# Optimization experiments

Hardware: AMD Instinct MI355X
Metric: run time of the kernel (lower is better)

The kernel has to match this reference:

```python
import jax, jax.numpy as jnp
import numpy as np

D = 512      # d_model
H = 8        # n_heads
NB = 6       # n_blocks
V = 32000    # vocab
F = 2048     # ff_size
B, L = 2, 1024
EPS = 1e-6
NEG = -1e10  # -INF used by create_causal_bias


def _ln(x, g, b):
    m = jnp.mean(x, axis=-1, keepdims=True)
    v = jnp.mean((x - m) ** 2, axis=-1, keepdims=True)
    return (x - m) * jax.lax.rsqrt(v + EPS) * g + b


def _split_heads(t):
    b, l, _ = t.shape
    return t.reshape(b, l, H, D // H).transpose(0, 2, 1, 3)  # [B,H,L,dh]


def _mha(q_in, kv_in, bias, wq, wk, wv, wo):
    # manual q@k^T / sqrt(dh) + bias -> softmax -> @v -> out proj (no bias terms)
    q = _split_heads(q_in @ wq)
    k = _split_heads(kv_in @ wk)
    v = _split_heads(kv_in @ wv)
    s = jnp.einsum('bhqd,bhkd->bhqk', q, k) / (D // H) ** 0.5 + bias
    a = jax.nn.softmax(s, axis=-1)
    o = jnp.einsum('bhqk,bhkd->bhqd', a, v)
    b_, _, l, _ = o.shape
    o = o.transpose(0, 2, 1, 3).reshape(b_, l, D)
    return o @ wo


def _pos_enc(length):
    pos = jnp.arange(length, dtype=jnp.float32)
    half = D // 2
    i = jnp.arange(half, dtype=jnp.float32)
    scaled = pos[:, None] / jnp.power(10000.0, i / half)[None]
    return jnp.concatenate([jnp.sin(scaled), jnp.cos(scaled)], axis=1)  # [L, D]


def setup_inputs() -> dict:
    key = jax.random.key(0)
    ks = jax.random.split(key, 16)
    s = 0.02
    inp = {
        'x': jax.random.randint(ks[0], (B, L), 0, V, dtype=jnp.int32),
        'ctx': jax.random.normal(ks[1], (B, L, D), jnp.float32),
        'emb': jax.random.normal(ks[2], (V, D), jnp.float32) * s,
        'wq_s': jax.random.normal(ks[3], (NB, D, D), jnp.float32) * s,
        'wk_s': jax.random.normal(ks[4], (NB, D, D), jnp.float32) * s,
        'wv_s': jax.random.normal(ks[5], (NB, D, D), jnp.float32) * s,
        'wo_s': jax.random.normal(ks[6], (NB, D, D), jnp.float32) * s,
        'wq_c': jax.random.normal(ks[7], (NB, D, D), jnp.float32) * s,
        'wk_c': jax.random.normal(ks[8], (NB, D, D), jnp.float32) * s,
        'wv_c': jax.random.normal(ks[9], (NB, D, D), jnp.float32) * s,
        'wo_c': jax.random.normal(ks[10], (NB, D, D), jnp.float32) * s,
        'w1': jax.random.normal(ks[11], (NB, D, F), jnp.float32) * s,
        'b1': jnp.zeros((NB, F), jnp.float32),
        'w2': jax.random.normal(ks[12], (NB, F, D), jnp.float32) * s,
        'b2': jnp.zeros((NB, D), jnp.float32),
        'ln1_g': jnp.ones((NB, D), jnp.float32), 'ln1_b': jnp.zeros((NB, D), jnp.float32),
        'ln2_g': jnp.ones((NB, D), jnp.float32), 'ln2_b': jnp.zeros((NB, D), jnp.float32),
        'ln3_g': jnp.ones((NB, D), jnp.float32), 'ln3_b': jnp.zeros((NB, D), jnp.float32),
        'lnf_g': jnp.ones((D,), jnp.float32), 'lnf_b': jnp.zeros((D,), jnp.float32),
    }
    return inp


def reference(x, ctx, emb, wq_s, wk_s, wv_s, wo_s, wq_c, wk_c, wv_c, wo_c,
              w1, b1, w2, b2, ln1_g, ln1_b, ln2_g, ln2_b, ln3_g, ln3_b,
              lnf_g, lnf_b):
    length = x.shape[1]
    # embedding * sqrt(D) + sinusoidal positional encoding
    h = emb[x] * jnp.sqrt(jnp.float32(D)) + _pos_enc(length)[None]
    # causal bias: upper triangle (excl. diag) filled with -INF, shape [1,1,L,L]
    causal = ((1.0 - jnp.tril(jnp.ones((length, length), jnp.float32))) * NEG)[None, None]
    zero_bias = jnp.zeros((1, 1, 1, 1), jnp.float32)  # no masking of encoder ctx
    for i in range(NB):
        y = _ln(h, ln1_g[i], ln1_b[i])
        h = h + _mha(y, y, causal, wq_s[i], wk_s[i], wv_s[i], wo_s[i])
        y = _ln(h, ln2_g[i], ln2_b[i])
        h = h + _mha(y, ctx, zero_bias, wq_c[i], wk_c[i], wv_c[i], wo_c[i])
        y = _ln(h, ln3_g[i], ln3_b[i])
        h = h + (jax.nn.relu(y @ w1[i] + b1[i]) @ w2[i] + b2[i])
    h = _ln(h, lnf_g, lnf_b)
    # emb2logits: shared embedding projection
    return jnp.einsum('bld,vd->blv', h, emb)
```

## Files before the change

### kernel.cpp

```cpp
#include <hip/hip_runtime.h>
#include <math.h>

#define Bv 2
#define Lv 1024
#define Dv 512
#define Hv 8
#define DH 64
#define Fv 2048
#define NBv 6
#define Vv 32000
#define Mv (Bv*Lv)
#define QS 1536
#define NEGINF -1e10f

typedef __attribute__((ext_vector_type(8))) short short8;
typedef __attribute__((ext_vector_type(4))) short short4v;
typedef __attribute__((ext_vector_type(4))) float floatx4;
typedef __attribute__((address_space(1))) const void gvoid;
typedef __attribute__((address_space(3))) void svoid;

__device__ __forceinline__ short f2bf(float f) {
    union { float f; unsigned u; } v; v.f = f;
    unsigned r = v.u + 0x7fffu + ((v.u >> 16) & 1u);
    return (short)(r >> 16);
}

__global__ __launch_bounds__(256)
void embed_kernel(const int* __restrict__ xi, const float* __restrict__ emb,
                  float* __restrict__ h)
{
    const int row = blockIdx.x;
    const int l   = row & (Lv - 1);
    const int tok = xi[row];
    const int tid = threadIdx.x;
#pragma unroll
    for (int s = 0; s < 2; ++s) {
        const int d  = tid + s * 256;
        const int dd = d & 255;
        const float freq = powf(10000.f, (float)dd * (1.f / 256.f));
        const float arg  = (float)l / freq;
        const float pe   = (d < 256) ? sinf(arg) : cosf(arg);
        h[(size_t)row * Dv + d] = emb[(size_t)tok * Dv + d] * 22.62741699796952f + pe;
    }
}

__global__ __launch_bounds__(256)
void cvt_kernel(const float* __restrict__ X, short* __restrict__ Y)
{
    const int i = (blockIdx.x * 256 + threadIdx.x) * 4;
    const float4 v = *(const float4*)(X + i);
    short4v p; p.x = f2bf(v.x); p.y = f2bf(v.y); p.z = f2bf(v.z); p.w = f2bf(v.w);
    *(short4v*)(Y + i) = p;
}

__global__ __launch_bounds__(256)
void ln_kernel(const float* __restrict__ X, const float* __restrict__ g,
               const float* __restrict__ bta, short* __restrict__ Y)
{
    const int row = blockIdx.x, tid = threadIdx.x;
    const float* xr = X + (size_t)row * Dv;
    const float x0 = xr[tid], x1 = xr[tid + 256];
    __shared__ float red[4];

    float s = x0 + x1;
#pragma unroll
    for (int off = 32; off; off >>= 1) s += __shfl_xor(s, off);
    if ((tid & 63) == 0) red[tid >> 6] = s;
    __syncthreads();
    const float mean = (red[0] + red[1] + red[2] + red[3]) * (1.f / Dv);
    __syncthreads();

    const float d0 = x0 - mean, d1 = x1 - mean;
    float v = d0 * d0 + d1 * d1;
#pragma unroll
    for (int off = 32; off; off >>= 1) v += __shfl_xor(v, off);
    if ((tid & 63) == 0) red[tid >> 6] = v;
    __syncthreads();
    const float var  = (red[0] + red[1] + red[2] + red[3]) * (1.f / Dv);
    const float rstd = rsqrtf(var + 1e-6f);

    Y[(size_t)row * Dv + tid]       = f2bf(d0 * rstd * g[tid]       + bta[tid]);
    Y[(size_t)row * Dv + tid + 256] = f2bf(d1 * rstd * g[tid + 256] + bta[tid + 256]);
}

template <int BM, int BN, int BK, int BMODE, bool OUTBF, bool SWZ>
__global__ __launch_bounds__(256)
void mgemm(const short* __restrict__ A, const float* __restrict__ B,
           void* __restrict__ Cp, int M, int N, int K,
           const float* __restrict__ bias,
           const float* __restrict__ residual, int relu)
{
    constexpr int WMT = BM / 2, MI = WMT / 16, NF = BN / 32;
    constexpr int CPR = BK / 8;
    __shared__ short As[BM * BK];
    __shared__ short Bs[BN * BK];
    const int tid  = threadIdx.x;
    const int wave = tid >> 6, lane = tid & 63;
    const int wm = wave & 1, wn = wave >> 1;
    const int quad = lane >> 4, l16 = lane & 15;

    int m0, n0;
    if (SWZ) {
        const int wg = (blockIdx.x & 7) * 500 + (blockIdx.x >> 3);
        m0 = (wg & 15) * BM;
        n0 = (wg >> 4) * BN;
    } else {
        m0 = blockIdx.y * BM;
        n0 = blockIdx.x * BN;
    }

    floatx4 acc[MI][NF];
#pragma unroll
    for (int i = 0; i < MI; ++i)
#pragma unroll
        for (int j = 0; j < NF; ++j)
            acc[i][j] = (floatx4){0.f, 0.f, 0.f, 0.f};

    for (int k0 = 0; k0 < K; k0 += BK) {
        __syncthreads();
#pragma unroll
        for (int s = 0; s < (BM * CPR) / 256; ++s) {
            const int c = s * 256 + tid;
            const int row = c / CPR, kp = (c % CPR) * 8;
            const int kps = kp ^ ((row & 7) << 3);
            const short* gp = A + (size_t)(m0 + row) * K + k0 + kps;
            __builtin_amdgcn_global_load_lds((gvoid*)gp, (svoid*)((char*)As + c * 16),
                                             16, 0, 0);
        }
        if (BMODE == 0) {
            constexpr int QN = BN / 4;
            constexpr int KSTEP = (256 / QN) * 4;
            const int qn  = tid % QN;
            const int kq0 = (tid / QN) * 4;
#pragma unroll
            for (int p = 0; p < BK / KSTEP; ++p) {
                const int krow = p * KSTEP + kq0;
                const float* gp = B + (size_t)(k0 + krow) * N + n0 + qn * 4;
                const float4 r0 = *(const float4*)(gp);
                const float4 r1 = *(const float4*)(gp + N);
                const float4 r2 = *(const float4*)(gp + 2 * (size_t)N);
                const float4 r3 = *(const float4*)(gp + 3 * (size_t)N);
#pragma unroll
                for (int e = 0; e < 4; ++e) {
                    const int n = qn * 4 + e;
                    short4v p4;
                    p4.x = f2bf(e == 0 ? r0.x : e == 1 ? r0.y : e == 2 ? r0.z : r0.w);
                    p4.y = f2bf(e == 0 ? r1.x : e == 1 ? r1.y : e == 2 ? r1.z : r1.w);
                    p4.z = f2bf(e == 0 ? r2.x : e == 1 ? r2.y : e == 2 ? r2.z : r2.w);
                    p4.w = f2bf(e == 0 ? r3.x : e == 1 ? r3.y : e == 2 ? r3.z : r3.w);
                    *(short4v*)&Bs[n * BK + (krow ^ ((n & 7) << 3))] = p4;
                }
            }
        } else if (BMODE == 1) {
#pragma unroll
            for (int f = 0; f < (BN * (BK / 4)) / 256; ++f) {
                const int gidx = f * 256 + tid;
                const int n = gidx / (BK / 4), q = (gidx % (BK / 4)) * 4;
                const float4 r = *(const float4*)(B + (size_t)(n0 + n) * K + k0 + q);
                short4v p; p.x = f2bf(r.x); p.y = f2bf(r.y); p.z = f2bf(r.z); p.w = f2bf(r.w);
                *(short4v*)&Bs[n * BK + (q ^ ((n & 7) << 3))] = p;
            }
        } else {
            const short* Bb = (const short*)B;
#pragma unroll
            for (int s = 0; s < (BN * CPR) / 256; ++s) {
                const int c = s * 256 + tid;
                const int row = c / CPR, kp = (c % CPR) * 8;
                const int kps = kp ^ ((row & 7) << 3);
                const short* gp = Bb + (size_t)(n0 + row) * K + k0 + kps;
                __builtin_amdgcn_global_load_lds((gvoid*)gp, (svoid*)((char*)Bs + c * 16),
                                                 16, 0, 0);
            }
        }
        __syncthreads();
#pragma unroll
        for (int kk = 0; kk < BK; kk += 32) {
            short8 af[MI];
#pragma unroll
            for (int mi = 0; mi < MI; ++mi) {
                const int r = wm * WMT + mi * 16 + l16;
                af[mi] = *(short8*)&As[r * BK + ((kk + quad * 8) ^ ((r & 7) << 3))];
            }
#pragma unroll
            for (int ni = 0; ni < NF; ++ni) {
                const int n = wn * (BN / 2) + ni * 16 + l16;
                const short8 bfr = *(short8*)&Bs[n * BK + ((kk + quad * 8) ^ ((n & 7) << 3))];
#pragma unroll
                for (int mi = 0; mi < MI; ++mi)
                    acc[mi][ni] = __builtin_amdgcn_mfma_f32_16x16x32_bf16(af[mi], bfr, acc[mi][ni], 0, 0, 0);
            }
        }
    }

#pragma unroll
    for (int mi = 0; mi < MI; ++mi)
#pragma unroll
        for (int ni = 0; ni < NF; ++ni)
#pragma unroll
            for (int r = 0; r < 4; ++r) {
                const int m = m0 + wm * WMT + mi * 16 + quad * 4 + r;
                const int n = n0 + wn * (BN / 2) + ni * 16 + l16;
                float v = acc[mi][ni][r];
                if (bias)     v += bias[n];
                if (residual) v += residual[(size_t)m * N + n];
                if (relu)     v = fmaxf(v, 0.f);
                if (OUTBF) ((short*)Cp)[(size_t)m * N + n] = f2bf(v);
                else       ((float*)Cp)[(size_t)m * N + n] = v;
            }
}

__global__ __launch_bounds__(256)
void qkv_gemm(const short* __restrict__ Aq, const short* __restrict__ Akv,
              const float* __restrict__ B0, const float* __restrict__ B1,
              const float* __restrict__ B2, short* __restrict__ QKV)
{
    constexpr int BM = 64, BN = 64, BK = 64, N = Dv, K = Dv;
    constexpr int WMT = BM / 2, MI = WMT / 16, NF = 2;
    constexpr int CPR = BK / 8;
    __shared__ short As[BM * BK];
    __shared__ short Bs[BN * BK];
    const int tid  = threadIdx.x;
    const int wave = tid >> 6, lane = tid & 63;
    const int wm = wave & 1, wn = wave >> 1;
    const int quad = lane >> 4, l16 = lane & 15;
    const int n0g = blockIdx.x * BN, m0 = blockIdx.y * BM;
    const int wsel = n0g >> 9, n0 = n0g & 511;
    const short* A = (wsel == 0) ? Aq : Akv;
    const float* B = (wsel == 0) ? B0 : (wsel == 1) ? B1 : B2;

    floatx4 acc[MI][NF];
#pragma unroll
    for (int i = 0; i < MI; ++i)
#pragma unroll
        for (int j = 0; j < NF; ++j)
            acc[i][j] = (floatx4){0.f, 0.f, 0.f, 0.f};

    for (int k0 = 0; k0 < K; k0 += BK) {
        __syncthreads();
#pragma unroll
        for (int s = 0; s < (BM * CPR) / 256; ++s) {
            const int c = s * 256 + tid;
            const int row = c / CPR, kp = (c % CPR) * 8;
            const int kps = kp ^ ((row & 7) << 3);
            const short* gp = A + (size_t)(m0 + row) * K + k0 + kps;
            __builtin_amdgcn_global_load_lds((gvoid*)gp, (svoid*)((char*)As + c * 16),
                                             16, 0, 0);
        }
        {
            constexpr int QN = BN / 4;
            const int qn  = tid % QN;
            const int krow = (tid / QN) * 4;
            const float* gp = B + (size_t)(k0 + krow) * N + n0 + qn * 4;
            const float4 r0 = *(const float4*)(gp);
            const float4 r1 = *(const float4*)(gp + N);
            const float4 r2 = *(const float4*)(gp + 2 * (size_t)N);
            const float4 r3 = *(const float4*)(gp + 3 * (size_t)N);
#pragma unroll
            for (int e = 0; e < 4; ++e) {
                const int n = qn * 4 + e;
                short4v p4;
                p4.x = f2bf(e == 0 ? r0.x : e == 1 ? r0.y : e == 2 ? r0.z : r0.w);
                p4.y = f2bf(e == 0 ? r1.x : e == 1 ? r1.y : e == 2 ? r1.z : r1.w);
                p4.z = f2bf(e == 0 ? r2.x : e == 1 ? r2.y : e == 2 ? r2.z : r2.w);
                p4.w = f2bf(e == 0 ? r3.x : e == 1 ? r3.y : e == 2 ? r3.z : r3.w);
                *(short4v*)&Bs[n * BK + (krow ^ ((n & 7) << 3))] = p4;
            }
        }
        __syncthreads();
#pragma unroll
        for (int kk = 0; kk < BK; kk += 32) {
            short8 af[MI];
#pragma unroll
            for (int mi = 0; mi < MI; ++mi) {
                const int r = wm * WMT + mi * 16 + l16;
                af[mi] = *(short8*)&As[r * BK + ((kk + quad * 8) ^ ((r & 7) << 3))];
            }
#pragma unroll
            for (int ni = 0; ni < NF; ++ni) {
                const int n = wn * 32 + ni * 16 + l16;
                const short8 bfr = *(short8*)&Bs[n * BK + ((kk + quad * 8) ^ ((n & 7) << 3))];
#pragma unroll
                for (int mi = 0; mi < MI; ++mi)
                    acc[mi][ni] = __builtin_amdgcn_mfma_f32_16x16x32_bf16(af[mi], bfr, acc[mi][ni], 0, 0, 0);
            }
        }
    }

#pragma unroll
    for (int mi = 0; mi < MI; ++mi)
#pragma unroll
        for (int ni = 0; ni < NF; ++ni)
#pragma unroll
            for (int r = 0; r < 4; ++r) {
                const int m = m0 + wm * WMT + mi * 16 + quad * 4 + r;
                const int n = n0g + wn * 32 + ni * 16 + l16;
                QKV[(size_t)m * QS + n] = f2bf(acc[mi][ni][r]);
            }
}

__global__ __launch_bounds__(256)
void attn_mfma(const short* __restrict__ QKV, short* __restrict__ Op, int causal)
{
    constexpr int PK = 72;
    __shared__ short Ks[64 * PK];
    __shared__ short Vs[64 * PK];
    __shared__ short Ps[4][16 * PK];
    const int tid  = threadIdx.x;
    const int wave = tid >> 6, lane = tid & 63;
    const int quad = lane >> 4, l16 = lane & 15;
    const int hh = blockIdx.y, bb = blockIdx.z;
    const int q0 = blockIdx.x * 64;
    const size_t base  = (size_t)bb * Lv * QS + (size_t)hh * DH;
    const short* Qp = QKV + base;
    const short* Kp = QKV + base + 512;
    const short* Vp = QKV + base + 1024;
    const size_t obase = (size_t)bb * Lv * Dv + (size_t)hh * DH;

    short8 aq[2];
    {
        const short* qp = Qp + (size_t)(q0 + wave * 16 + l16) * QS + quad * 8;
        aq[0] = *(const short8*)qp;
        aq[1] = *(const short8*)(qp + 32);
    }

    floatx4 o[4];
#pragma unroll
    for (int i = 0; i < 4; ++i) o[i] = (floatx4){0.f, 0.f, 0.f, 0.f};
    float mrow[4] = {-3.4e38f, -3.4e38f, -3.4e38f, -3.4e38f};
    float srow[4] = {0.f, 0.f, 0.f, 0.f};

    const int ntiles = causal ? (q0 / 64 + 1) : (Lv / 64);

    for (int t = 0; t < ntiles; ++t) {
        const int j0 = t * 64;
        __syncthreads();
#pragma unroll
        for (int s = 0; s < 2; ++s) {
            const int c = s * 256 + tid;
            const int j = c >> 3, off = (c & 7) * 8;
            const size_t grow = (size_t)(j0 + j) * QS + off;
            *(short8*)&Ks[j * PK + off] = *(const short8*)(Kp + grow);
            const short8 v = *(const short8*)(Vp + grow);
            const int jx = j ^ ((c & 7) << 3);
#pragma unroll
            for (int e = 0; e < 8; ++e)
                Vs[(off + e) * PK + jx] = v[e];
        }
        __syncthreads();

        floatx4 sf[4];
#pragma unroll
        for (int nf = 0; nf < 4; ++nf) {
            const short8 bk0 = *(const short8*)&Ks[(nf * 16 + l16) * PK + quad * 8];
            const short8 bk1 = *(const short8*)&Ks[(nf * 16 + l16) * PK + 32 + quad * 8];
            floatx4 z = (floatx4){0.f, 0.f, 0.f, 0.f};
            z = __builtin_amdgcn_mfma_f32_16x16x32_bf16(aq[0], bk0, z, 0, 0, 0);
            z = __builtin_amdgcn_mfma_f32_16x16x32_bf16(aq[1], bk1, z, 0, 0, 0);
            sf[nf] = z;
        }

        const bool mask = causal && (j0 == q0);
#pragma unroll
        for (int nf = 0; nf < 4; ++nf) {
            const int jabs = j0 + nf * 16 + l16;
#pragma unroll
            for (int r = 0; r < 4; ++r) {
                float v = sf[nf][r] * 0.125f;
                if (mask && jabs > q0 + wave * 16 + quad * 4 + r) v = NEGINF;
                sf[nf][r] = v;
            }
        }

#pragma unroll
        for (int r = 0; r < 4; ++r) {
            float v = fmaxf(fmaxf(sf[0][r], sf[1][r]), fmaxf(sf[2][r], sf[3][r]));
            v = fmaxf(v, __shfl_xor(v, 1));
            v = fmaxf(v, __shfl_xor(v, 2));
            v = fmaxf(v, __shfl_xor(v, 4));
            v = fmaxf(v, __shfl_xor(v, 8));
            const float mnew = fmaxf(mrow[r], v);
            const float corr = __expf(mrow[r] - mnew);
            mrow[r] = mnew;
            srow[r] *= corr;
#pragma unroll
            for (int nf = 0; nf < 4; ++nf) o[nf][r] *= corr;
        }

#pragma unroll
        for (int nf = 0; nf < 4; ++nf) {
#pragma unroll
            for (int r = 0; r < 4; ++r) {
                const float pv = __expf(sf[nf][r] - mrow[r]);
                srow[r] += pv;
                Ps[wave][(quad * 4 + r) * PK + nf * 16 + l16] = f2bf(pv);
            }
        }
        __builtin_amdgcn_wave_barrier();

        const short8 pa0 = *(const short8*)&Ps[wave][l16 * PK + quad * 8];
        const short8 pa1 = *(const short8*)&Ps[wave][l16 * PK + 32 + quad * 8];
#pragma unroll
        for (int nf = 0; nf < 4; ++nf) {
            const int d   = nf * 16 + l16;
            const int swz = ((d >> 3) & 7) << 3;
            const short8 bv0 = *(const short8*)&Vs[d * PK + ((quad * 8) ^ swz)];
            const short8 bv1 = *(const short8*)&Vs[d * PK + ((32 + quad * 8) ^ swz)];
            o[nf] = __builtin_amdgcn_mfma_f32_16x16x32_bf16(pa0, bv0, o[nf], 0, 0, 0);
            o[nf] = __builtin_amdgcn_mfma_f32_16x16x32_bf16(pa1, bv1, o[nf], 0, 0, 0);
        }
    }

#pragma unroll
    for (int r = 0; r < 4; ++r) {
        float s = srow[r];
        s += __shfl_xor(s, 1);
        s += __shfl_xor(s, 2);
        s += __shfl_xor(s, 4);
        s += __shfl_xor(s, 8);
        srow[r] = 1.f / s;
    }
#pragma unroll
    for (int nf = 0; nf < 4; ++nf)
#pragma unroll
        for (int r = 0; r < 4; ++r) {
            const size_t addr = obase + (size_t)(q0 + wave * 16 + quad * 4 + r) * Dv
                              + nf * 16 + l16;
            Op[addr] = f2bf(o[nf][r] * srow[r]);
        }
}

extern "C" void kernel_launch(void* const* d_in, const int* in_sizes, int n_in,
                              void* d_out, int out_size, void* d_ws, size_t ws_size,
                              hipStream_t stream)
{
    const int*   x    = (const int*)  d_in[0];
    const float* ctx  = (const float*)d_in[1];
    const float* emb  = (const float*)d_in[2];
    const float* wq_s = (const float*)d_in[3];
    const float* wk_s = (const float*)d_in[4];
    const float* wv_s = (const float*)d_in[5];
    const float* wo_s = (const float*)d_in[6];
    const float* wq_c = (const float*)d_in[7];
    const float* wk_c = (const float*)d_in[8];
    const float* wv_c = (const float*)d_in[9];
    const float* wo_c = (const float*)d_in[10];
    const float* w1   = (const float*)d_in[11];
    const float* b1   = (const float*)d_in[12];
    const float* w2   = (const float*)d_in[13];
    const float* b2   = (const float*)d_in[14];
    const float* ln1g = (const float*)d_in[15];
    const float* ln1b = (const float*)d_in[16];
    const float* ln2g = (const float*)d_in[17];
    const float* ln2b = (const float*)d_in[18];
    const float* ln3g = (const float*)d_in[19];
    const float* ln3b = (const float*)d_in[20];
    const float* lnfg = (const float*)d_in[21];
    const float* lnfb = (const float*)d_in[22];
    float* out = (float*)d_out;

    char* wsb = (char*)d_ws;
    float* h      = (float*)(wsb);
    short* y_bf   = (short*)(wsb + (4u  << 20));
    short* ao_bf  = (short*)(wsb + (6u  << 20));
    short* ctx_bf = (short*)(wsb + (8u  << 20));
    short* qkv    = (short*)(wsb + (10u << 20));
    short* ff_bf  = (short*)(wsb + (10u << 20));
    short* emb_bf = (short*)(wsb + (18u << 20));
    const bool fastv = ws_size >= (52u << 20);

    const dim3 blk(256);
    const dim3 gAttn(Lv / 64, Hv, Bv);
    const dim3 gQKV(QS / 64, Mv / 64);
    const dim3 gD(Dv / 64, Mv / 32);
    const dim3 gF(Fv / 128, Mv / 64);
    const dim3 gV(16 * 250);

    embed_kernel<<<Mv, blk, 0, stream>>>(x, emb, h);
    cvt_kernel<<<(Mv * Dv) / 1024, blk, 0, stream>>>(ctx, ctx_bf);
    if (fastv)
        cvt_kernel<<<(Vv * Dv) / 1024, blk, 0, stream>>>(emb, emb_bf);

    for (int i = 0; i < NBv; ++i) {
        const size_t wOff = (size_t)i * Dv * Dv;
        ln_kernel<<<Mv, blk, 0, stream>>>(h, ln1g + i * Dv, ln1b + i * Dv, y_bf);
        qkv_gemm<<<gQKV, blk, 0, stream>>>(y_bf, y_bf,
                                           wq_s + wOff, wk_s + wOff, wv_s + wOff, qkv);
        attn_mfma<<<gAttn, blk, 0, stream>>>(qkv, ao_bf, 1);
        mgemm<32, 64, 64, 0, false, false><<<gD, blk, 0, stream>>>(ao_bf, wo_s + wOff, h,
                                                                   Mv, Dv, Dv, nullptr, h, 0);
        ln_kernel<<<Mv, blk, 0, stream>>>(h, ln2g + i * Dv, ln2b + i * Dv, y_bf);
        qkv_gemm<<<gQKV, blk, 0, stream>>>(y_bf, ctx_bf,
                                           wq_c + wOff, wk_c + wOff, wv_c + wOff, qkv);
        attn_mfma<<<gAttn, blk, 0, stream>>>(qkv, ao_bf, 0);
        mgemm<32, 64, 64, 0, false, false><<<gD, blk, 0, stream>>>(ao_bf, wo_c + wOff, h,
                                                                   Mv, Dv, Dv, nullptr, h, 0);
        ln_kernel<<<Mv, blk, 0, stream>>>(h, ln3g + i * Dv, ln3b + i * Dv, y_bf);
        mgemm<64, 128, 64, 0, true, false><<<gF, blk, 0, stream>>>(y_bf, w1 + (size_t)i * Dv * Fv,
                                                                   ff_bf, Mv, Fv, Dv,
                                                                   b1 + (size_t)i * Fv, nullptr, 1);
        mgemm<32, 64, 64, 0, false, false><<<gD, blk, 0, stream>>>(ff_bf, w2 + (size_t)i * Fv * Dv,
                                                                   h, Mv, Dv, Fv,
                                                                   b2 + (size_t)i * Dv, h, 0);
    }

    ln_kernel<<<Mv, blk, 0, stream>>>(h, lnfg, lnfb, y_bf);
    if (fastv)
        mgemm<128, 128, 64, 2, false, true><<<gV, blk, 0, stream>>>(y_bf, (const float*)emb_bf,
                                                                    out, Mv, Vv, Dv,
                                                                    nullptr, nullptr, 0);
    else
        mgemm<128, 128, 64, 1, false, true><<<gV, blk, 0, stream>>>(y_bf, emb, out,
                                                                    Mv, Vv, Dv,
                                                                    nullptr, nullptr, 0);
}
```

Before: 1.671 ms.

## Pre-transpose weights to bf16, batch cross-attention KV projection, double-buffer GEMM loads

When the workspace is large enough, all weights are converted once per call to transposed bf16, so every GEMM uses the direct global-to-LDS bf16 load path instead of converting fp32 B tiles in-kernel. The cross-attention K/V projections for all six blocks are computed in one large GEMM up front, since ctx does not change between blocks. The bf16 path also gains a double-buffered LDS pipeline that overlaps the next tile's loads with MFMA compute. The cost is extra transpose launches each call and a much larger workspace, and if the workspace is too small the old path runs instead.

```diff
diff --git a/kernel.cpp b/kernel.cpp
--- a/kernel.cpp
+++ b/kernel.cpp
@@ -11,6 +11,7 @@
 #define Vv 32000
 #define Mv (Bv*Lv)
 #define QS 1536
+#define KVS 6144
 #define NEGINF -1e10f
 
 typedef __attribute__((ext_vector_type(8))) short short8;
@@ -54,6 +55,35 @@
 }
 
 __global__ __launch_bounds__(256)
+void tr_cvt(const float* __restrict__ src, short* __restrict__ dst,
+            int K, int N, size_t dstZ, size_t dstOff)
+{
+    __shared__ float t[64][65];
+    const int z  = blockIdx.z;
+    const int n0 = blockIdx.x * 64, k0 = blockIdx.y * 64;
+    const int tid = threadIdx.x;
+    const float* s = src + (size_t)z * K * N;
+    short* d = dst + (size_t)z * dstZ + dstOff;
+
+    const int kr = tid >> 2, nc = (tid & 3) * 16;
+#pragma unroll
+    for (int j = 0; j < 16; j += 4) {
+        const float4 v = *(const float4*)(s + (size_t)(k0 + kr) * N + n0 + nc + j);
+        t[kr][nc + j + 0] = v.x; t[kr][nc + j + 1] = v.y;
+        t[kr][nc + j + 2] = v.z; t[kr][nc + j + 3] = v.w;
+    }
+    __syncthreads();
+    const int nr = tid >> 2, kc = (tid & 3) * 16;
+    short8 o0, o1;
+#pragma unroll
+    for (int j = 0; j < 8; ++j)  o0[j] = f2bf(t[kc + j][nr]);
+#pragma unroll
+    for (int j = 0; j < 8; ++j)  o1[j] = f2bf(t[kc + 8 + j][nr]);
+    *(short8*)(d + (size_t)(n0 + nr) * K + k0 + kc)     = o0;
+    *(short8*)(d + (size_t)(n0 + nr) * K + k0 + kc + 8) = o1;
+}
+
+__global__ __launch_bounds__(256)
 void ln_kernel(const float* __restrict__ X, const float* __restrict__ g,
                const float* __restrict__ bta, short* __restrict__ Y)
 {
@@ -83,7 +113,7 @@
     Y[(size_t)row * Dv + tid + 256] = f2bf(d1 * rstd * g[tid + 256] + bta[tid + 256]);
 }
 
-template <int BM, int BN, int BK, int BMODE, bool OUTBF, bool SWZ>
+template <int BM, int BN, int BK, int BMODE, bool OUTBF, bool SWZ, bool DBUF>
 __global__ __launch_bounds__(256)
 void mgemm(const short* __restrict__ A, const float* __restrict__ B,
            void* __restrict__ Cp, int M, int N, int K,
@@ -92,8 +122,9 @@
 {
     constexpr int WMT = BM / 2, MI = WMT / 16, NF = BN / 32;
     constexpr int CPR = BK / 8;
-    __shared__ short As[BM * BK];
-    __shared__ short Bs[BN * BK];
+    constexpr int NBUF = (DBUF && BMODE == 2) ? 2 : 1;
+    __shared__ short As[NBUF * BM * BK];
+    __shared__ short Bs[NBUF * BN * BK];
     const int tid  = threadIdx.x;
     const int wave = tid >> 6, lane = tid & 63;
     const int wm = wave & 1, wn = wave >> 1;
@@ -116,79 +147,116 @@
         for (int j = 0; j < NF; ++j)
             acc[i][j] = (floatx4){0.f, 0.f, 0.f, 0.f};
 
-    for (int k0 = 0; k0 < K; k0 += BK) {
-        __syncthreads();
-#pragma unroll
-        for (int s = 0; s < (BM * CPR) / 256; ++s) {
-            const int c = s * 256 + tid;
-            const int row = c / CPR, kp = (c % CPR) * 8;
-            const int kps = kp ^ ((row & 7) << 3);
-            const short* gp = A + (size_t)(m0 + row) * K + k0 + kps;
-            __builtin_amdgcn_global_load_lds((gvoid*)gp, (svoid*)((char*)As + c * 16),
-                                             16, 0, 0);
-        }
-        if (BMODE == 0) {
-            constexpr int QN = BN / 4;
-            constexpr int KSTEP = (256 / QN) * 4;
-            const int qn  = tid % QN;
-            const int kq0 = (tid / QN) * 4;
-#pragma unroll
-            for (int p = 0; p < BK / KSTEP; ++p) {
-                const int krow = p * KSTEP + kq0;
-                const float* gp = B + (size_t)(k0 + krow) * N + n0 + qn * 4;
-                const float4 r0 = *(const float4*)(gp);
-                const float4 r1 = *(const float4*)(gp + N);
-                const float4 r2 = *(const float4*)(gp + 2 * (size_t)N);
-                const float4 r3 = *(const float4*)(gp + 3 * (size_t)N);
-#pragma unroll
-                for (int e = 0; e < 4; ++e) {
-                    const int n = qn * 4 + e;
-                    short4v p4;
-                    p4.x = f2bf(e == 0 ? r0.x : e == 1 ? r0.y : e == 2 ? r0.z : r0.w);
-                    p4.y = f2bf(e == 0 ? r1.x : e == 1 ? r1.y : e == 2 ? r1.z : r1.w);
-                    p4.z = f2bf(e == 0 ? r2.x : e == 1 ? r2.y : e == 2 ? r2.z : r2.w);
-                    p4.w = f2bf(e == 0 ? r3.x : e == 1 ? r3.y : e == 2 ? r3.z : r3.w);
-                    *(short4v*)&Bs[n * BK + (krow ^ ((n & 7) << 3))] = p4;
-                }
-            }
-        } else if (BMODE == 1) {
-#pragma unroll
-            for (int f = 0; f < (BN * (BK / 4)) / 256; ++f) {
-                const int gidx = f * 256 + tid;
-                const int n = gidx / (BK / 4), q = (gidx % (BK / 4)) * 4;
-                const float4 r = *(const float4*)(B + (size_t)(n0 + n) * K + k0 + q);
-                short4v p; p.x = f2bf(r.x); p.y = f2bf(r.y); p.z = f2bf(r.z); p.w = f2bf(r.w);
-                *(short4v*)&Bs[n * BK + (q ^ ((n & 7) << 3))] = p;
-            }
-        } else {
-            const short* Bb = (const short*)B;
+    auto computeTile = [&](const short* Asb, const short* Bsb) {
+#pragma unroll
+        for (int kk = 0; kk < BK; kk += 32) {
+            short8 af[MI];
+#pragma unroll
+            for (int mi = 0; mi < MI; ++mi) {
+                const int r = wm * WMT + mi * 16 + l16;
+                af[mi] = *(const short8*)&Asb[r * BK + ((kk + quad * 8) ^ ((r & 7) << 3))];
+            }
+#pragma unroll
+            for (int ni = 0; ni < NF; ++ni) {
+                const int n = wn * (BN / 2) + ni * 16 + l16;
+                const short8 bfr = *(const short8*)&Bsb[n * BK + ((kk + quad * 8) ^ ((n & 7) << 3))];
+#pragma unroll
+                for (int mi = 0; mi < MI; ++mi)
+                    acc[mi][ni] = __builtin_amdgcn_mfma_f32_16x16x32_bf16(af[mi], bfr, acc[mi][ni], 0, 0, 0);
+            }
+        }
+    };
+
+    if constexpr (DBUF && BMODE == 2) {
+        const short* Bb = (const short*)B;
+        auto stage = [&](int buf, int kbase) {
+#pragma unroll
+            for (int s = 0; s < (BM * CPR) / 256; ++s) {
+                const int c = s * 256 + tid;
+                const int row = c / CPR, kp = (c % CPR) * 8;
+                const int kps = kp ^ ((row & 7) << 3);
+                const short* gp = A + (size_t)(m0 + row) * K + kbase + kps;
+                __builtin_amdgcn_global_load_lds((gvoid*)gp,
+                    (svoid*)((char*)As + buf * (BM * BK * 2) + c * 16), 16, 0, 0);
+            }
 #pragma unroll
             for (int s = 0; s < (BN * CPR) / 256; ++s) {
                 const int c = s * 256 + tid;
                 const int row = c / CPR, kp = (c % CPR) * 8;
                 const int kps = kp ^ ((row & 7) << 3);
-                const short* gp = Bb + (size_t)(n0 + row) * K + k0 + kps;
-                __builtin_amdgcn_global_load_lds((gvoid*)gp, (svoid*)((char*)Bs + c * 16),
+                const short* gp = Bb + (size_t)(n0 + row) * K + kbase + kps;
+                __builtin_amdgcn_global_load_lds((gvoid*)gp,
+                    (svoid*)((char*)Bs + buf * (BN * BK * 2) + c * 16), 16, 0, 0);
+            }
+        };
+        stage(0, 0);
+        __syncthreads();
+        const int NT = K / BK;
+        for (int t = 0; t < NT; ++t) {
+            const int cur = t & 1;
+            if (t + 1 < NT) stage(cur ^ 1, (t + 1) * BK);
+            computeTile(As + cur * BM * BK, Bs + cur * BN * BK);
+            __syncthreads();
+        }
+    } else {
+        for (int k0 = 0; k0 < K; k0 += BK) {
+            __syncthreads();
+#pragma unroll
+            for (int s = 0; s < (BM * CPR) / 256; ++s) {
+                const int c = s * 256 + tid;
+                const int row = c / CPR, kp = (c % CPR) * 8;
+                const int kps = kp ^ ((row & 7) << 3);
+                const short* gp = A + (size_t)(m0 + row) * K + k0 + kps;
+                __builtin_amdgcn_global_load_lds((gvoid*)gp, (svoid*)((char*)As + c * 16),
                                                  16, 0, 0);
             }
-        }
-        __syncthreads();
-#pragma unroll
-        for (int kk = 0; kk < BK; kk += 32) {
-            short8 af[MI];
-#pragma unroll
-            for (int mi = 0; mi < MI; ++mi) {
-                const int r = wm * WMT + mi * 16 + l16;
-                af[mi] = *(short8*)&As[r * BK + ((kk + quad * 8) ^ ((r & 7) << 3))];
-            }
-#pragma unroll
-            for (int ni = 0; ni < NF; ++ni) {
-                const int n = wn * (BN / 2) + ni * 16 + l16;
-                const short8 bfr = *(short8*)&Bs[n * BK + ((kk + quad * 8) ^ ((n & 7) << 3))];
-#pragma unroll
-                for (int mi = 0; mi < MI; ++mi)
-                    acc[mi][ni] = __builtin_amdgcn_mfma_f32_16x16x32_bf16(af[mi], bfr, acc[mi][ni], 0, 0, 0);
-            }
+            if (BMODE == 0) {
+                constexpr int QN = BN / 4;
+                constexpr int KSTEP = (256 / QN) * 4;
+                const int qn  = tid % QN;
+                const int kq0 = (tid / QN) * 4;
+#pragma unroll
+                for (int p = 0; p < BK / KSTEP; ++p) {
+                    const int krow = p * KSTEP + kq0;
+                    const float* gp = B + (size_t)(k0 + krow) * N + n0 + qn * 4;
+                    const float4 r0 = *(const float4*)(gp);
+                    const float4 r1 = *(const float4*)(gp + N);
+                    const float4 r2 = *(const float4*)(gp + 2 * (size_t)N);
+                    const float4 r3 = *(const float4*)(gp + 3 * (size_t)N);
+#pragma unroll
+                    for (int e = 0; e < 4; ++e) {
+                        const int n = qn * 4 + e;
+                        short4v p4;
+                        p4.x = f2bf(e == 0 ? r0.x : e == 1 ? r0.y : e == 2 ? r0.z : r0.w);
+                        p4.y = f2bf(e == 0 ? r1.x : e == 1 ? r1.y : e == 2 ? r1.z : r1.w);
+                        p4.z = f2bf(e == 0 ? r2.x : e == 1 ? r2.y : e == 2 ? r2.z : r2.w);
+                        p4.w = f2bf(e == 0 ? r3.x : e == 1 ? r3.y : e == 2 ? r3.z : r3.w);
+                        *(short4v*)&Bs[n * BK + (krow ^ ((n & 7) << 3))] = p4;
+                    }
+                }
+            } else if (BMODE == 1) {
+#pragma unroll
+                for (int f = 0; f < (BN * (BK / 4)) / 256; ++f) {
+                    const int gidx = f * 256 + tid;
+                    const int n = gidx / (BK / 4), q = (gidx % (BK / 4)) * 4;
+                    const float4 r = *(const float4*)(B + (size_t)(n0 + n) * K + k0 + q);
+                    short4v p; p.x = f2bf(r.x); p.y = f2bf(r.y); p.z = f2bf(r.z); p.w = f2bf(r.w);
+                    *(short4v*)&Bs[n * BK + (q ^ ((n & 7) << 3))] = p;
+                }
+            } else {
+                const short* Bb = (const short*)B;
+#pragma unroll
+                for (int s = 0; s < (BN * CPR) / 256; ++s) {
+                    const int c = s * 256 + tid;
+                    const int row = c / CPR, kp = (c % CPR) * 8;
+                    const int kps = kp ^ ((row & 7) << 3);
+                    const short* gp = Bb + (size_t)(n0 + row) * K + k0 + kps;
+                    __builtin_amdgcn_global_load_lds((gvoid*)gp, (svoid*)((char*)Bs + c * 16),
+                                                     16, 0, 0);
+                }
+            }
+            __syncthreads();
+            computeTile(As, Bs);
         }
     }
 
@@ -299,7 +367,9 @@
 }
 
 __global__ __launch_bounds__(256)
-void attn_mfma(const short* __restrict__ QKV, short* __restrict__ Op, int causal)
+void attn_mfma(const short* __restrict__ Qp, int qstr,
+               const short* __restrict__ Kp, const short* __restrict__ Vp, int kvstr,
+               short* __restrict__ Op, int causal)
 {
     constexpr int PK = 72;
     __shared__ short Ks[64 * PK];
@@ -310,15 +380,13 @@
     const int quad = lane >> 4, l16 = lane & 15;
     const int hh = blockIdx.y, bb = blockIdx.z;
     const int q0 = blockIdx.x * 64;
-    const size_t base  = (size_t)bb * Lv * QS + (size_t)hh * DH;
-    const short* Qp = QKV + base;
-    const short* Kp = QKV + base + 512;
-    const short* Vp = QKV + base + 1024;
-    const size_t obase = (size_t)bb * Lv * Dv + (size_t)hh * DH;
+    const size_t qbase  = (size_t)bb * Lv * qstr  + (size_t)hh * DH;
+    const size_t kvbase = (size_t)bb * Lv * kvstr + (size_t)hh * DH;
+    const size_t obase  = (size_t)bb * Lv * Dv + (size_t)hh * DH;
 
     short8 aq[2];
     {
-        const short* qp = Qp + (size_t)(q0 + wave * 16 + l16) * QS + quad * 8;
+        const short* qp = Qp + qbase + (size_t)(q0 + wave * 16 + l16) * qstr + quad * 8;
         aq[0] = *(const short8*)qp;
         aq[1] = *(const short8*)(qp + 32);
     }
@@ -338,7 +406,7 @@
         for (int s = 0; s < 2; ++s) {
             const int c = s * 256 + tid;
             const int j = c >> 3, off = (c & 7) * 8;
-            const size_t grow = (size_t)(j0 + j) * QS + off;
+            const size_t grow = kvbase + (size_t)(j0 + j) * kvstr + off;
             *(short8*)&Ks[j * PK + off] = *(const short8*)(Kp + grow);
             const short8 v = *(const short8*)(Vp + grow);
             const int jx = j ^ ((c & 7) << 3);
@@ -459,57 +527,134 @@
     float* out = (float*)d_out;
 
     char* wsb = (char*)d_ws;
-    float* h      = (float*)(wsb);
-    short* y_bf   = (short*)(wsb + (4u  << 20));
-    short* ao_bf  = (short*)(wsb + (6u  << 20));
-    short* ctx_bf = (short*)(wsb + (8u  << 20));
-    short* qkv    = (short*)(wsb + (10u << 20));
-    short* ff_bf  = (short*)(wsb + (10u << 20));
-    short* emb_bf = (short*)(wsb + (18u << 20));
-    const bool fastv = ws_size >= (52u << 20);
-
     const dim3 blk(256);
     const dim3 gAttn(Lv / 64, Hv, Bv);
-    const dim3 gQKV(QS / 64, Mv / 64);
-    const dim3 gD(Dv / 64, Mv / 32);
-    const dim3 gF(Fv / 128, Mv / 64);
     const dim3 gV(16 * 250);
 
-    embed_kernel<<<Mv, blk, 0, stream>>>(x, emb, h);
-    cvt_kernel<<<(Mv * Dv) / 1024, blk, 0, stream>>>(ctx, ctx_bf);
-    if (fastv)
+    if (ws_size >= (150u << 20)) {
+        float* h      = (float*)(wsb);
+        short* y_bf   = (short*)(wsb + (4u   << 20));
+        short* ao_bf  = (short*)(wsb + (6u   << 20));
+        short* ctx_bf = (short*)(wsb + (8u   << 20));
+        short* qkv    = (short*)(wsb + (10u  << 20));
+        short* ff_bf  = (short*)(wsb + (16u  << 20));
+        short* qb     = (short*)(wsb + (24u  << 20));
+        short* kvc    = (short*)(wsb + (26u  << 20));
+        short* wqkv_s = (short*)(wsb + (50u  << 20));
+        short* wo_s_t = (short*)(wsb + (60u  << 20));
+        short* wq_c_t = (short*)(wsb + (64u  << 20));
+        short* wo_c_t = (short*)(wsb + (68u  << 20));
+        short* kvw    = (short*)(wsb + (72u  << 20));
+        short* w1t    = (short*)(wsb + (79u  << 20));
+        short* w2t    = (short*)(wsb + (92u  << 20));
+        short* emb_bf = (short*)(wsb + (105u << 20));
+
+        embed_kernel<<<Mv, blk, 0, stream>>>(x, emb, h);
+        cvt_kernel<<<(Mv * Dv) / 1024, blk, 0, stream>>>(ctx, ctx_bf);
         cvt_kernel<<<(Vv * Dv) / 1024, blk, 0, stream>>>(emb, emb_bf);
 
-    for (int i = 0; i < NBv; ++i) {
-        const size_t wOff = (size_t)i * Dv * Dv;
-        ln_kernel<<<Mv, blk, 0, stream>>>(h, ln1g + i * Dv, ln1b + i * Dv, y_bf);
-        qkv_gemm<<<gQKV, blk, 0, stream>>>(y_bf, y_bf,
-                                           wq_s + wOff, wk_s + wOff, wv_s + wOff, qkv);
-        attn_mfma<<<gAttn, blk, 0, stream>>>(qkv, ao_bf, 1);
-        mgemm<32, 64, 64, 0, false, false><<<gD, blk, 0, stream>>>(ao_bf, wo_s + wOff, h,
-                                                                   Mv, Dv, Dv, nullptr, h, 0);
-        ln_kernel<<<Mv, blk, 0, stream>>>(h, ln2g + i * Dv, ln2b + i * Dv, y_bf);
-        qkv_gemm<<<gQKV, blk, 0, stream>>>(y_bf, ctx_bf,
-                                           wq_c + wOff, wk_c + wOff, wv_c + wOff, qkv);
-        attn_mfma<<<gAttn, blk, 0, stream>>>(qkv, ao_bf, 0);
-        mgemm<32, 64, 64, 0, false, false><<<gD, blk, 0, stream>>>(ao_bf, wo_c + wOff, h,
-                                                                   Mv, Dv, Dv, nullptr, h, 0);
-        ln_kernel<<<Mv, blk, 0, stream>>>(h, ln3g + i * Dv, ln3b + i * Dv, y_bf);
-        mgemm<64, 128, 64, 0, true, false><<<gF, blk, 0, stream>>>(y_bf, w1 + (size_t)i * Dv * Fv,
-                                                                   ff_bf, Mv, Fv, Dv,
-                                                                   b1 + (size_t)i * Fv, nullptr, 1);
-        mgemm<32, 64, 64, 0, false, false><<<gD, blk, 0, stream>>>(ff_bf, w2 + (size_t)i * Fv * Dv,
-                                                                   h, Mv, Dv, Fv,
-                                                                   b2 + (size_t)i * Dv, h, 0);
-    }
-
-    ln_kernel<<<Mv, blk, 0, stream>>>(h, lnfg, lnfb, y_bf);
-    if (fastv)
-        mgemm<128, 128, 64, 2, false, true><<<gV, blk, 0, stream>>>(y_bf, (const float*)emb_bf,
-                                                                    out, Mv, Vv, Dv,
-                                                                    nullptr, nullptr, 0);
-    else
-        mgemm<128, 128, 64, 1, false, true><<<gV, blk, 0, stream>>>(y_bf, emb, out,
-                                                                    Mv, Vv, Dv,
-                                                                    nullptr, nullptr, 0);
-}
+        const dim3 gT55(8, 8, NBv);
+        const dim3 gT5F(Fv / 64, 8, NBv);
+        const dim3 gTF5(8, Fv / 64, NBv);
+        tr_cvt<<<gT55, blk, 0, stream>>>(wq_s, wqkv_s, Dv, Dv, (size_t)QS * Dv, 0);
+        tr_cvt<<<gT55, blk, 0, stream>>>(wk_s, wqkv_s, Dv, Dv, (size_t)QS * Dv, (size_t)Dv * Dv);
+        tr_cvt<<<gT55, blk, 0, stream>>>(wv_s, wqkv_s, Dv, Dv, (size_t)QS * Dv, (size_t)2 * Dv * Dv);
+        tr_cvt<<<gT55, blk, 0, stream>>>(wo_s, wo_s_t, Dv, Dv, (size_t)Dv * Dv, 0);
+        tr_cvt<<<gT55, blk, 0, stream>>>(wq_c, wq_c_t, Dv, Dv, (size_t)Dv * Dv, 0);
+        tr_cvt<<<gT55, blk, 0, stream>>>(wo_c, wo_c_t, Dv, Dv, (size_t)Dv * Dv, 0);
+        tr_cvt<<<gT55, blk, 0, stream>>>(wk_c, kvw, Dv, Dv, (size_t)2 * Dv * Dv, 0);
+        tr_cvt<<<gT55, blk, 0, stream>>>(wv_c, kvw, Dv, Dv, (size_t)2 * Dv * Dv, (size_t)Dv * Dv);
+        tr_cvt<<<gT5F, blk, 0, stream>>>(w1, w1t, Dv, Fv, (size_t)Fv * Dv, 0);
+        tr_cvt<<<gTF5, blk, 0, stream>>>(w2, w2t, Fv, Dv, (size_t)Dv * Fv, 0);
+
+        {
+            const dim3 g(KVS / 64, Mv / 128);
+            mgemm<128, 64, 64, 2, true, false, true><<<g, blk, 0, stream>>>(
+                ctx_bf, (const float*)kvw, kvc, Mv, KVS, Dv, nullptr, nullptr, 0);
+        }
+
+        const dim3 gQKV(QS / 64, Mv / 64);
+        const dim3 gD(Dv / 64, Mv / 32);
+        const dim3 gF1(Fv / 128, Mv / 64);
+
+        for (int i = 0; i < NBv; ++i) {
+            ln_kernel<<<Mv, blk, 0, stream>>>(h, ln1g + i * Dv, ln1b + i * Dv, y_bf);
+            mgemm<64, 64, 64, 2, true, false, true><<<gQKV, blk, 0, stream>>>(
+                y_bf, (const float*)(wqkv_s + (size_t)i * QS * Dv), qkv,
+                Mv, QS, Dv, nullptr, nullptr, 0);
+            attn_mfma<<<gAttn, blk, 0, stream>>>(qkv, QS, qkv + 512, qkv + 1024, QS, ao_bf, 1);
+            mgemm<32, 64, 64, 2, false, false, true><<<gD, blk, 0, stream>>>(
+                ao_bf, (const float*)(wo_s_t + (size_t)i * Dv * Dv), h,
+                Mv, Dv, Dv, nullptr, h, 0);
+            ln_kernel<<<Mv, blk, 0, stream>>>(h, ln2g + i * Dv, ln2b + i * Dv, y_bf);
+            mgemm<32, 64, 64, 2, true, false, true><<<gD, blk, 0, stream>>>(
+                y_bf, (const float*)(wq_c_t + (size_t)i * Dv * Dv), qb,
+                Mv, Dv, Dv, nullptr, nullptr, 0);
+            attn_mfma<<<gAttn, blk, 0, stream>>>(qb, Dv,
+                kvc + (size_t)i * 1024, kvc + (size_t)i * 1024 + 512, KVS, ao_bf, 0);
+            mgemm<32, 64, 64, 2, false, false, true><<<gD, blk, 0, stream>>>(
+                ao_bf, (const float*)(wo_c_t + (size_t)i * Dv * Dv), h,
+                Mv, Dv, Dv, nullptr, h, 0);
+            ln_kernel<<<Mv, blk, 0, stream>>>(h, ln3g + i * Dv, ln3b + i * Dv, y_bf);
+            mgemm<64, 128, 64, 2, true, false, true><<<gF1, blk, 0, stream>>>(
+                y_bf, (const float*)(w1t + (size_t)i * Fv * Dv), ff_bf,
+                Mv, Fv, Dv, b1 + (size_t)i * Fv, nullptr, 1);
+            mgemm<32, 64, 64, 2, false, false, true><<<gD, blk, 0, stream>>>(
+                ff_bf, (const float*)(w2t + (size_t)i * Dv * Fv), h,
+                Mv, Dv, Fv, b2 + (size_t)i * Dv, h, 0);
+        }
+
+        ln_kernel<<<Mv, blk, 0, stream>>>(h, lnfg, lnfb, y_bf);
+        mgemm<128, 128, 64, 2, false, true, false><<<gV, blk, 0, stream>>>(
+            y_bf, (const float*)emb_bf, out, Mv, Vv, Dv, nullptr, nullptr, 0);
+    } else {
+        float* h      = (float*)(wsb);
+        short* y_bf   = (short*)(wsb + (4u  << 20));
+        short* ao_bf  = (short*)(wsb + (6u  << 20));
+        short* ctx_bf = (short*)(wsb + (8u  << 20));
+        short* qkv    = (short*)(wsb + (10u << 20));
+        short* ff_bf  = (short*)(wsb + (10u << 20));
+        short* emb_bf = (short*)(wsb + (18u << 20));
+        const bool fastv = ws_size >= (52u << 20);
+
+        const dim3 gQKV(QS / 64, Mv / 64);
+        const dim3 gD(Dv / 64, Mv / 32);
+        const dim3 gF(Fv / 128, Mv / 64);
+
+        embed_kernel<<<Mv, blk, 0, stream>>>(x, emb, h);
+        cvt_kernel<<<(Mv * Dv) / 1024, blk, 0, stream>>>(ctx, ctx_bf);
+        if (fastv)
+            cvt_kernel<<<(Vv * Dv) / 1024, blk, 0, stream>>>(emb, emb_bf);
+
+        for (int i = 0; i < NBv; ++i) {
+            const size_t wOff = (size_t)i * Dv * Dv;
+            ln_kernel<<<Mv, blk, 0, stream>>>(h, ln1g + i * Dv, ln1b + i * Dv, y_bf);
+            qkv_gemm<<<gQKV, blk, 0, stream>>>(y_bf, y_bf,
+                                               wq_s + wOff, wk_s + wOff, wv_s + wOff, qkv);
+            attn_mfma<<<gAttn, blk, 0, stream>>>(qkv, QS, qkv + 512, qkv + 1024, QS, ao_bf, 1);
+            mgemm<32, 64, 64, 0, false, false, false><<<gD, blk, 0, stream>>>(
+                ao_bf, wo_s + wOff, h, Mv, Dv, Dv, nullptr, h, 0);
+            ln_kernel<<<Mv, blk, 0, stream>>>(h, ln2g + i * Dv, ln2b + i * Dv, y_bf);
+            qkv_gemm<<<gQKV, blk, 0, stream>>>(y_bf, ctx_bf,
+                                               wq_c + wOff, wk_c + wOff, wv_c + wOff, qkv);
+            attn_mfma<<<gAttn, blk, 0, stream>>>(qkv, QS, qkv + 512, qkv + 1024, QS, ao_bf, 0);
+            mgemm<32, 64, 64, 0, false, false, false><<<gD, blk, 0, stream>>>(
+                ao_bf, wo_c + wOff, h, Mv, Dv, Dv, nullptr, h, 0);
+            ln_kernel<<<Mv, blk, 0, stream>>>(h, ln3g + i * Dv, ln3b + i * Dv, y_bf);
+            mgemm<64, 128, 64, 0, true, false, false><<<gF, blk, 0, stream>>>(
+                y_bf, w1 + (size_t)i * Dv * Fv, ff_bf, Mv, Fv, Dv,
+                b1 + (size_t)i * Fv, nullptr, 1);
+            mgemm<32, 64, 64, 0, false, false, false><<<gD, blk, 0, stream>>>(
+                ff_bf, w2 + (size_t)i * Fv * Dv, h, Mv, Dv, Fv,
+                b2 + (size_t)i * Dv, h, 0);
+        }
+
+        ln_kernel<<<Mv, blk, 0, stream>>>(h, lnfg, lnfb, y_bf);
+        if (fastv)
+            mgemm<128, 128, 64, 2, false, true, false><<<gV, blk, 0, stream>>>(
+                y_bf, (const float*)emb_bf, out, Mv, Vv, Dv, nullptr, nullptr, 0);
+        else
+            mgemm<128, 128, 64, 1, false, true, false><<<gV, blk, 0, stream>>>(
+                y_bf, emb, out, Mv, Vv, Dv, nullptr, nullptr, 0);
+    }
+}
```

Measured after the change: 1.407 ms. 1.19x faster.
